# Kernel optimization log

Measured on AMD Instinct MI355X. Metric: run time of the kernel, lower is better.

Reference implementation:

```python
import jax, jax.numpy as jnp
import numpy as np

E = 1024
H = 16
HD = E // H
SCALE = HD ** -0.5


def setup_inputs() -> dict:
    key = jax.random.key(0)
    ks = jax.random.split(key, 8)
    B, S = 2, 2048
    query = jax.random.normal(ks[0], (B, S, E), dtype=jnp.float32)
    kk = jax.random.normal(ks[1], (B, S, E), dtype=jnp.float32)
    vv = jax.random.normal(ks[2], (B, S, E), dtype=jnp.float32)
    lim_in = 1.0 / np.sqrt(E)
    in_proj_w = jax.random.uniform(ks[3], (3 * E, E), minval=-lim_in, maxval=lim_in, dtype=jnp.float32)
    in_proj_b = jax.random.uniform(ks[4], (3 * E,), minval=-lim_in, maxval=lim_in, dtype=jnp.float32)
    out_proj_w = jax.random.uniform(ks[5], (E, E), minval=-lim_in, maxval=lim_in, dtype=jnp.float32)
    out_proj_b = jax.random.uniform(ks[6], (E,), minval=-lim_in, maxval=lim_in, dtype=jnp.float32)
    return {
        "query": query, "key": kk, "value": vv,
        "in_proj_w": in_proj_w, "in_proj_b": in_proj_b,
        "out_proj_w": out_proj_w, "out_proj_b": out_proj_b,
    }


def reference(query, key, value, in_proj_w, in_proj_b, out_proj_w, out_proj_b):
    # NOTE: the torch module ignores `key`/`value`; q,k,v all come from in_proj(query).
    B, S, _ = query.shape
    qkv = jnp.einsum('bse,fe->bsf', query, in_proj_w) + in_proj_b  # [B,S,3E]
    q, k, v = jnp.split(qkv, 3, axis=-1)
    # [B,H,S,HD]
    q = q.reshape(B, S, H, HD).transpose(0, 2, 1, 3) * SCALE
    k = k.reshape(B, S, H, HD).transpose(0, 2, 1, 3)
    v = v.reshape(B, S, H, HD).transpose(0, 2, 1, 3)
    scores = jnp.einsum('bhqd,bhkd->bhqk', q, k)  # [B,H,S,S]
    attn_weights = jax.nn.softmax(scores, axis=-1)
    attn_out = jnp.einsum('bhqk,bhkd->bhqd', attn_weights, v)
    attn_out = attn_out.transpose(0, 2, 1, 3).reshape(B, S, E)
    out = jnp.einsum('bse,fe->bsf', attn_out, out_proj_w) + out_proj_b
    return out, attn_weights
```

## Files before the change

kernel.cpp:

```cpp
#include <hip/hip_runtime.h>

constexpr int kB = 2;
constexpr int kS = 2048;
constexpr int kE = 1024;
constexpr int kF = 3 * kE;

typedef __attribute__((ext_vector_type(8))) short short8;
typedef __attribute__((ext_vector_type(4))) float f32x4;

__device__ __forceinline__ ushort f2bf_rne(float f) {
    uint u = __float_as_uint(f);
    return (ushort)((u + 0x7FFF + ((u >> 16) & 1)) >> 16);
}

__global__ __launch_bounds__(256) void k_cast(const float* __restrict__ in,
                                              ushort* __restrict__ out, int n4)
{
    int i = blockIdx.x * 256 + threadIdx.x;
    if (i < n4) {
        float4 v = ((const float4*)in)[i];
        ushort4 o;
        o.x = f2bf_rne(v.x); o.y = f2bf_rne(v.y);
        o.z = f2bf_rne(v.z); o.w = f2bf_rne(v.w);
        ((ushort4*)out)[i] = o;
    }
}

__device__ __forceinline__ void stage64(ushort* __restrict__ Ls,
                                        const ushort* __restrict__ g,
                                        int gstride, int tid)
{
    int r = tid >> 3;
    int c = (tid & 7) << 3;
    *(uint4*)(Ls + r * 72 + c)        = *(const uint4*)(g + (size_t)r * gstride + c);
    *(uint4*)(Ls + (r + 32) * 72 + c) = *(const uint4*)(g + (size_t)(r + 32) * gstride + c);
}

#define FRAG72(Ls, row, koff) (*(const short8*)((Ls) + (size_t)(row) * 72 + (koff)))

__global__ __launch_bounds__(256) void k_gemm(const ushort* __restrict__ A,
                                              const ushort* __restrict__ Bw,
                                              const float* __restrict__ bias,
                                              ushort* __restrict__ Cb,
                                              float* __restrict__ Cf,
                                              int K, int ldc, int qcols)
{
    __shared__ ushort As[128 * 40];
    __shared__ ushort Bs[128 * 40];
    const int tid = threadIdx.x;
    const int wave = tid >> 6, lane = tid & 63;
    const int quad = lane >> 4, c16 = lane & 15;
    const int wm = (wave >> 1) * 64, wn = (wave & 1) * 64;
    const int row0 = blockIdx.y * 128, col0 = blockIdx.x * 128;

    f32x4 acc[4][4];
#pragma unroll
    for (int i = 0; i < 4; ++i)
#pragma unroll
        for (int j = 0; j < 4; ++j) acc[i][j] = (f32x4){0.f, 0.f, 0.f, 0.f};

    const int sr = tid >> 2;
    const int sq = (tid & 3) << 3;

    for (int k0 = 0; k0 < K; k0 += 32) {
        __syncthreads();
        *(uint4*)(As + sr * 40 + sq)        = *(const uint4*)(A + (size_t)(row0 + sr) * K + k0 + sq);
        *(uint4*)(As + (sr + 64) * 40 + sq) = *(const uint4*)(A + (size_t)(row0 + sr + 64) * K + k0 + sq);
        *(uint4*)(Bs + sr * 40 + sq)        = *(const uint4*)(Bw + (size_t)(col0 + sr) * K + k0 + sq);
        *(uint4*)(Bs + (sr + 64) * 40 + sq) = *(const uint4*)(Bw + (size_t)(col0 + sr + 64) * K + k0 + sq);
        __syncthreads();

        short8 af[4], bf[4];
#pragma unroll
        for (int mt = 0; mt < 4; ++mt)
            af[mt] = *(const short8*)(As + (size_t)(wm + mt * 16 + c16) * 40 + quad * 8);
#pragma unroll
        for (int nt = 0; nt < 4; ++nt)
            bf[nt] = *(const short8*)(Bs + (size_t)(wn + nt * 16 + c16) * 40 + quad * 8);
#pragma unroll
        for (int mt = 0; mt < 4; ++mt)
#pragma unroll
            for (int nt = 0; nt < 4; ++nt)
                acc[mt][nt] = __builtin_amdgcn_mfma_f32_16x16x32_bf16(af[mt], bf[nt], acc[mt][nt], 0, 0, 0);
    }

#pragma unroll
    for (int nt = 0; nt < 4; ++nt) {
        const int colg = col0 + wn + nt * 16 + c16;
        const float bv = bias[colg];
        const float sc = (colg < qcols) ? 0.125f : 1.0f;
#pragma unroll
        for (int mt = 0; mt < 4; ++mt)
#pragma unroll
            for (int r = 0; r < 4; ++r) {
                const int rowg = row0 + wm + mt * 16 + quad * 4 + r;
                float v = acc[mt][nt][r] + bv;
                if (Cb) Cb[(size_t)rowg * ldc + colg] = f2bf_rne(v * sc);
                else    Cf[(size_t)rowg * ldc + colg] = v;
            }
    }
}

__global__ __launch_bounds__(256) void k_vt(const ushort* __restrict__ qkvb,
                                            ushort* __restrict__ vT)
{
    const int b = blockIdx.z, si = blockIdx.y, di = blockIdx.x;
    __shared__ ushort Ls[64 * 72];
    const int tid = threadIdx.x;
    stage64(Ls, qkvb + ((size_t)(b * kS + si * 64)) * kF + 2 * kE + di * 64, kF, tid);
    __syncthreads();
    const int dd = tid >> 3;
    const int s8 = (tid & 7) << 3;
#pragma unroll
    for (int it = 0; it < 2; ++it) {
        const int d = dd + it * 32;
        uint o[4];
#pragma unroll
        for (int i = 0; i < 4; ++i) {
            uint lo = Ls[(s8 + 2 * i) * 72 + d];
            uint hi = Ls[(s8 + 2 * i + 1) * 72 + d];
            o[i] = lo | (hi << 16);
        }
        *(uint4*)(vT + ((size_t)(b * kE + di * 64 + d)) * kS + si * 64 + s8) = *(uint4*)o;
    }
}

__global__ __launch_bounds__(256) void k_attn(const ushort* __restrict__ qkvb,
                                              const ushort* __restrict__ vT,
                                              float* __restrict__ wts,
                                              ushort* __restrict__ aob)
{
    __shared__ ushort Qs[64 * 72];
    __shared__ ushort Ks[64 * 72];
    __shared__ ushort Vts[64 * 72];
    __shared__ ushort Ps[64 * 72];

    const int tid = threadIdx.x;
    const int wave = tid >> 6, lane = tid & 63;
    const int quad = lane >> 4, c16 = lane & 15;
    const int z = blockIdx.y;
    const int b = z >> 4, h = z & 15;
    const int Rq = blockIdx.x * 64;

    const ushort* qg  = qkvb + ((size_t)(b * kS + Rq)) * kF + h * 64;
    const ushort* kg  = qkvb + ((size_t)b * kS) * kF + kE + h * 64;
    const ushort* vtg = vT + ((size_t)(b * kE + h * 64)) * kS;
    float* wrow = wts + ((size_t)(z * kS) + Rq + wave * 16) * kS;

    stage64(Qs, qg, kF, tid);
    __syncthreads();
    const short8 qa0 = FRAG72(Qs, wave * 16 + c16, quad * 8);
    const short8 qa1 = FRAG72(Qs, wave * 16 + c16, quad * 8 + 32);

    float m[4] = {-1e30f, -1e30f, -1e30f, -1e30f};
    float l[4] = {0.f, 0.f, 0.f, 0.f};

    for (int j = 0; j < 32; ++j) {
        __syncthreads();
        stage64(Ks, kg + (size_t)j * 64 * kF, kF, tid);
        __syncthreads();
        f32x4 s[4];
#pragma unroll
        for (int ct = 0; ct < 4; ++ct) {
            short8 b0 = FRAG72(Ks, ct * 16 + c16, quad * 8);
            short8 b1 = FRAG72(Ks, ct * 16 + c16, quad * 8 + 32);
            f32x4 a = (f32x4){0.f, 0.f, 0.f, 0.f};
            a = __builtin_amdgcn_mfma_f32_16x16x32_bf16(qa0, b0, a, 0, 0, 0);
            a = __builtin_amdgcn_mfma_f32_16x16x32_bf16(qa1, b1, a, 0, 0, 0);
            s[ct] = a;
        }
#pragma unroll
        for (int r = 0; r < 4; ++r) {
            float tm = fmaxf(fmaxf(s[0][r], s[1][r]), fmaxf(s[2][r], s[3][r]));
            tm = fmaxf(tm, __shfl_xor(tm, 1));
            tm = fmaxf(tm, __shfl_xor(tm, 2));
            tm = fmaxf(tm, __shfl_xor(tm, 4));
            tm = fmaxf(tm, __shfl_xor(tm, 8));
            const float mn = fmaxf(m[r], tm);
            float sum = __expf(s[0][r] - mn) + __expf(s[1][r] - mn)
                      + __expf(s[2][r] - mn) + __expf(s[3][r] - mn);
            sum += __shfl_xor(sum, 1);
            sum += __shfl_xor(sum, 2);
            sum += __shfl_xor(sum, 4);
            sum += __shfl_xor(sum, 8);
            l[r] = l[r] * __expf(m[r] - mn) + sum;
            m[r] = mn;
        }
    }
    float invl[4];
#pragma unroll
    for (int r = 0; r < 4; ++r) invl[r] = 1.0f / l[r];

    f32x4 o[4];
#pragma unroll
    for (int i = 0; i < 4; ++i) o[i] = (f32x4){0.f, 0.f, 0.f, 0.f};

    for (int j = 0; j < 32; ++j) {
        __syncthreads();
        stage64(Ks, kg + (size_t)j * 64 * kF, kF, tid);
        stage64(Vts, vtg + j * 64, kS, tid);
        __syncthreads();
        f32x4 s[4];
#pragma unroll
        for (int ct = 0; ct < 4; ++ct) {
            short8 b0 = FRAG72(Ks, ct * 16 + c16, quad * 8);
            short8 b1 = FRAG72(Ks, ct * 16 + c16, quad * 8 + 32);
            f32x4 a = (f32x4){0.f, 0.f, 0.f, 0.f};
            a = __builtin_amdgcn_mfma_f32_16x16x32_bf16(qa0, b0, a, 0, 0, 0);
            a = __builtin_amdgcn_mfma_f32_16x16x32_bf16(qa1, b1, a, 0, 0, 0);
            s[ct] = a;
        }
#pragma unroll
        for (int ct = 0; ct < 4; ++ct)
#pragma unroll
            for (int r = 0; r < 4; ++r) {
                const float p = __expf(s[ct][r] - m[r]) * invl[r];
                wrow[(size_t)(quad * 4 + r) * kS + j * 64 + ct * 16 + c16] = p;
                Ps[(size_t)(wave * 16 + quad * 4 + r) * 72 + ct * 16 + c16] = f2bf_rne(p);
            }
        __syncthreads();
        const short8 pa0 = FRAG72(Ps, wave * 16 + c16, quad * 8);
        const short8 pa1 = FRAG72(Ps, wave * 16 + c16, quad * 8 + 32);
#pragma unroll
        for (int ct2 = 0; ct2 < 4; ++ct2) {
            short8 v0 = FRAG72(Vts, ct2 * 16 + c16, quad * 8);
            short8 v1 = FRAG72(Vts, ct2 * 16 + c16, quad * 8 + 32);
            o[ct2] = __builtin_amdgcn_mfma_f32_16x16x32_bf16(pa0, v0, o[ct2], 0, 0, 0);
            o[ct2] = __builtin_amdgcn_mfma_f32_16x16x32_bf16(pa1, v1, o[ct2], 0, 0, 0);
        }
    }

#pragma unroll
    for (int ct2 = 0; ct2 < 4; ++ct2)
#pragma unroll
        for (int r = 0; r < 4; ++r) {
            const size_t row = (size_t)(b * kS + Rq + wave * 16 + quad * 4 + r);
            aob[row * kE + h * 64 + ct2 * 16 + c16] = f2bf_rne(o[ct2][r]);
        }
}


extern "C" void kernel_launch(void* const* d_in, const int* in_sizes, int n_in,
                              void* d_out, int out_size, void* d_ws, size_t ws_size,
                              hipStream_t stream)
{
    const float* query = (const float*)d_in[0];
    const float* in_w  = (const float*)d_in[3];
    const float* in_b  = (const float*)d_in[4];
    const float* out_w = (const float*)d_in[5];
    const float* out_b = (const float*)d_in[6];

    float* out = (float*)d_out;
    float* wts = out + (size_t)kB * kS * kE;

    constexpr size_t MB = 1u << 20;
    char* w = (char*)d_ws;
    ushort* qbf  = (ushort*)(w);
    ushort* wbfi = (ushort*)(w + 8 * MB);
    ushort* wbfo = (ushort*)(w + 14 * MB);
    ushort* qkvb = (ushort*)(w + 16 * MB);
    ushort* vT   = (ushort*)(w + 40 * MB);
    ushort* aob  = (ushort*)(w + 48 * MB);

    dim3 blk(256);
    k_cast<<<dim3((4096 * 1024 / 4 + 255) / 256), blk, 0, stream>>>(query, qbf, 4096 * 1024 / 4);
    k_cast<<<dim3((3072 * 1024 / 4 + 255) / 256), blk, 0, stream>>>(in_w, wbfi, 3072 * 1024 / 4);
    k_cast<<<dim3((1024 * 1024 / 4 + 255) / 256), blk, 0, stream>>>(out_w, wbfo, 1024 * 1024 / 4);

    k_gemm<<<dim3(kF / 128, 4096 / 128), blk, 0, stream>>>(qbf, wbfi, in_b, qkvb, nullptr, kE, kF, kE);

    k_vt<<<dim3(16, 32, 2), blk, 0, stream>>>(qkvb, vT);

    k_attn<<<dim3(kS / 64, kB * 16), blk, 0, stream>>>(qkvb, vT, wts, aob);

    k_gemm<<<dim3(kE / 128, 4096 / 128), blk, 0, stream>>>(aob, wbfo, out_b, nullptr, out, kE, kE, 0);
}
```

Measured before the change: 862.3 us.

## Cache full score rows in LDS to avoid recomputing QK^T in attention

The attention kernel now processes 32 query rows per 512-thread block and stores the whole 32x2048 bf16 score row block in LDS, so QK^T is computed once instead of twice. Softmax runs in a separate exp pass over LDS, and K/V tiles are double-buffered. Weights are written from the stored bf16 exponentials with a fixed offset. This removes the redundant score recompute and the per-tile online max/sum shuffles, at the cost of about 140 KB of LDS per block (one block per CU) and bf16 rounding of the stored scores and weights.

After: 1.013 ms. 17.5% more time.

```diff
diff --git a/kernel.cpp b/kernel.cpp
--- a/kernel.cpp
+++ b/kernel.cpp
@@ -11,6 +11,9 @@
 __device__ __forceinline__ ushort f2bf_rne(float f) {
     uint u = __float_as_uint(f);
     return (ushort)((u + 0x7FFF + ((u >> 16) & 1)) >> 16);
+}
+__device__ __forceinline__ float bf2f(ushort u) {
+    return __uint_as_float((uint)u << 16);
 }
 
 __global__ __launch_bounds__(256) void k_cast(const float* __restrict__ in,
@@ -36,8 +39,6 @@
     *(uint4*)(Ls + (r + 32) * 72 + c) = *(const uint4*)(g + (size_t)(r + 32) * gstride + c);
 }
 
-#define FRAG72(Ls, row, koff) (*(const short8*)((Ls) + (size_t)(row) * 72 + (koff)))
-
 __global__ __launch_bounds__(256) void k_gemm(const ushort* __restrict__ A,
                                               const ushort* __restrict__ Bw,
                                               const float* __restrict__ bias,
@@ -125,118 +126,153 @@
     }
 }
 
-__global__ __launch_bounds__(256) void k_attn(const ushort* __restrict__ qkvb,
+constexpr int SP = 2056;
+constexpr int SC_SH = 32 * SP;
+constexpr int KB_SH = 64 * 72;
+constexpr int ATTN_LDS_BYTES = (SC_SH + 2 * KB_SH) * 2 + (32 * 4 + 32) * 4;
+
+__global__ __launch_bounds__(512) void k_attn(const ushort* __restrict__ qkvb,
                                               const ushort* __restrict__ vT,
                                               float* __restrict__ wts,
                                               ushort* __restrict__ aob)
 {
-    __shared__ ushort Qs[64 * 72];
-    __shared__ ushort Ks[64 * 72];
-    __shared__ ushort Vts[64 * 72];
-    __shared__ ushort Ps[64 * 72];
-
-    const int tid = threadIdx.x;
+    extern __shared__ ushort smem[];
+    ushort* Sc  = smem;
+    ushort* Kb0 = Sc + SC_SH;
+    ushort* Kb1 = Kb0 + KB_SH;
+    float* maxscr = (float*)(Kb1 + KB_SH);
+    float* invls  = maxscr + 32 * 4;
+
+    const int tid  = threadIdx.x;
     const int wave = tid >> 6, lane = tid & 63;
     const int quad = lane >> 4, c16 = lane & 15;
     const int z = blockIdx.y;
     const int b = z >> 4, h = z & 15;
-    const int Rq = blockIdx.x * 64;
+    const int Rq = blockIdx.x * 32;
+    const int mb = (wave & 1) * 16;
+    const int nb = (wave >> 1) * 16;
 
     const ushort* qg  = qkvb + ((size_t)(b * kS + Rq)) * kF + h * 64;
     const ushort* kg  = qkvb + ((size_t)b * kS) * kF + kE + h * 64;
     const ushort* vtg = vT + ((size_t)(b * kE + h * 64)) * kS;
-    float* wrow = wts + ((size_t)(z * kS) + Rq + wave * 16) * kS;
-
-    stage64(Qs, qg, kF, tid);
-    __syncthreads();
-    const short8 qa0 = FRAG72(Qs, wave * 16 + c16, quad * 8);
-    const short8 qa1 = FRAG72(Qs, wave * 16 + c16, quad * 8 + 32);
-
-    float m[4] = {-1e30f, -1e30f, -1e30f, -1e30f};
-    float l[4] = {0.f, 0.f, 0.f, 0.f};
-
+
+    const int strow = tid >> 3, stcol = (tid & 7) << 3;
+
+    const short8 qa0 = *(const short8*)(qg + (size_t)(mb + c16) * kF + quad * 8);
+    const short8 qa1 = *(const short8*)(qg + (size_t)(mb + c16) * kF + quad * 8 + 32);
+
+    constexpr float Coff = 3.0f;
+    float m4[4] = {-1e30f, -1e30f, -1e30f, -1e30f};
+
+    *(uint4*)(Kb0 + strow * 72 + stcol) = *(const uint4*)(kg + (size_t)strow * kF + stcol);
+    __syncthreads();
+
+#pragma unroll 2
     for (int j = 0; j < 32; ++j) {
+        const ushort* cur = (j & 1) ? Kb1 : Kb0;
+        ushort* nxt       = (j & 1) ? Kb0 : Kb1;
+        if (j + 1 < 32)
+            *(uint4*)(nxt + strow * 72 + stcol) =
+                *(const uint4*)(kg + (size_t)((j + 1) * 64 + strow) * kF + stcol);
+
+        short8 b0 = *(const short8*)(cur + (size_t)(nb + c16) * 72 + quad * 8);
+        short8 b1 = *(const short8*)(cur + (size_t)(nb + c16) * 72 + quad * 8 + 32);
+        f32x4 a = (f32x4){0.f, 0.f, 0.f, 0.f};
+        a = __builtin_amdgcn_mfma_f32_16x16x32_bf16(qa0, b0, a, 0, 0, 0);
+        a = __builtin_amdgcn_mfma_f32_16x16x32_bf16(qa1, b1, a, 0, 0, 0);
+#pragma unroll
+        for (int r = 0; r < 4; ++r) {
+            const float t = a[r] - Coff;
+            m4[r] = fmaxf(m4[r], t);
+            Sc[(size_t)(mb + quad * 4 + r) * SP + j * 64 + nb + c16] = f2bf_rne(t);
+        }
         __syncthreads();
-        stage64(Ks, kg + (size_t)j * 64 * kF, kF, tid);
+    }
+
+#pragma unroll
+    for (int r = 0; r < 4; ++r) {
+        float t = m4[r];
+        t = fmaxf(t, __shfl_xor(t, 1));
+        t = fmaxf(t, __shfl_xor(t, 2));
+        t = fmaxf(t, __shfl_xor(t, 4));
+        t = fmaxf(t, __shfl_xor(t, 8));
+        if (c16 == 0) maxscr[(mb + quad * 4 + r) * 4 + (wave >> 1)] = t;
+    }
+    __syncthreads();
+
+    const int prow = wave * 4 + (lane >> 4);
+    const float mt = fmaxf(fmaxf(maxscr[prow * 4 + 0], maxscr[prow * 4 + 1]),
+                           fmaxf(maxscr[prow * 4 + 2], maxscr[prow * 4 + 3]));
+    float ls0 = 0.f, ls1 = 0.f;
+    ushort* rbase = Sc + (size_t)prow * SP + c16 * 8;
+#pragma unroll 4
+    for (int it = 0; it < 16; ++it) {
+        short8 sv = *(const short8*)(rbase + it * 128);
+        short8 ev;
+#pragma unroll
+        for (int i = 0; i < 8; ++i) {
+            const float e = __expf(bf2f((ushort)sv[i]) - mt);
+            if (i & 1) ls1 += e; else ls0 += e;
+            ev[i] = (short)f2bf_rne(e);
+        }
+        *(short8*)(rbase + it * 128) = ev;
+    }
+    float lsum = ls0 + ls1;
+    lsum += __shfl_xor(lsum, 1);
+    lsum += __shfl_xor(lsum, 2);
+    lsum += __shfl_xor(lsum, 4);
+    lsum += __shfl_xor(lsum, 8);
+    if (c16 == 0) invls[prow] = 1.0f / lsum;
+    __syncthreads();
+
+    const float invl_m = invls[mb + c16];
+    f32x4 o = (f32x4){0.f, 0.f, 0.f, 0.f};
+
+    *(uint4*)(Kb0 + strow * 72 + stcol) = *(const uint4*)(vtg + (size_t)strow * kS + stcol);
+    __syncthreads();
+
+#pragma unroll 2
+    for (int j = 0; j < 32; ++j) {
+        const ushort* cur = (j & 1) ? Kb1 : Kb0;
+        ushort* nxt       = (j & 1) ? Kb0 : Kb1;
+        if (j + 1 < 32)
+            *(uint4*)(nxt + strow * 72 + stcol) =
+                *(const uint4*)(vtg + (size_t)strow * kS + (j + 1) * 64 + stcol);
+
+        const ushort* pr = Sc + (size_t)(mb + c16) * SP + j * 64 + quad * 8;
+        short8 pa0 = *(const short8*)(pr);
+        short8 pa1 = *(const short8*)(pr + 32);
+        short8 v0 = *(const short8*)(cur + (size_t)(nb + c16) * 72 + quad * 8);
+        short8 v1 = *(const short8*)(cur + (size_t)(nb + c16) * 72 + quad * 8 + 32);
+        o = __builtin_amdgcn_mfma_f32_16x16x32_bf16(pa0, v0, o, 0, 0, 0);
+        o = __builtin_amdgcn_mfma_f32_16x16x32_bf16(pa1, v1, o, 0, 0, 0);
+
+        if (wave < 2) {
+            float* wp = wts + ((size_t)z * kS + Rq + mb + c16) * kS + j * 64 + quad * 8;
+            float4 w0, w1, w2, w3;
+            w0.x = bf2f((ushort)pa0[0]) * invl_m; w0.y = bf2f((ushort)pa0[1]) * invl_m;
+            w0.z = bf2f((ushort)pa0[2]) * invl_m; w0.w = bf2f((ushort)pa0[3]) * invl_m;
+            w1.x = bf2f((ushort)pa0[4]) * invl_m; w1.y = bf2f((ushort)pa0[5]) * invl_m;
+            w1.z = bf2f((ushort)pa0[6]) * invl_m; w1.w = bf2f((ushort)pa0[7]) * invl_m;
+            w2.x = bf2f((ushort)pa1[0]) * invl_m; w2.y = bf2f((ushort)pa1[1]) * invl_m;
+            w2.z = bf2f((ushort)pa1[2]) * invl_m; w2.w = bf2f((ushort)pa1[3]) * invl_m;
+            w3.x = bf2f((ushort)pa1[4]) * invl_m; w3.y = bf2f((ushort)pa1[5]) * invl_m;
+            w3.z = bf2f((ushort)pa1[6]) * invl_m; w3.w = bf2f((ushort)pa1[7]) * invl_m;
+            *(float4*)(wp)      = w0;
+            *(float4*)(wp + 4)  = w1;
+            *(float4*)(wp + 32) = w2;
+            *(float4*)(wp + 36) = w3;
+        }
         __syncthreads();
-        f32x4 s[4];
-#pragma unroll
-        for (int ct = 0; ct < 4; ++ct) {
-            short8 b0 = FRAG72(Ks, ct * 16 + c16, quad * 8);
-            short8 b1 = FRAG72(Ks, ct * 16 + c16, quad * 8 + 32);
-            f32x4 a = (f32x4){0.f, 0.f, 0.f, 0.f};
-            a = __builtin_amdgcn_mfma_f32_16x16x32_bf16(qa0, b0, a, 0, 0, 0);
-            a = __builtin_amdgcn_mfma_f32_16x16x32_bf16(qa1, b1, a, 0, 0, 0);
-            s[ct] = a;
-        }
-#pragma unroll
-        for (int r = 0; r < 4; ++r) {
-            float tm = fmaxf(fmaxf(s[0][r], s[1][r]), fmaxf(s[2][r], s[3][r]));
-            tm = fmaxf(tm, __shfl_xor(tm, 1));
-            tm = fmaxf(tm, __shfl_xor(tm, 2));
-            tm = fmaxf(tm, __shfl_xor(tm, 4));
-            tm = fmaxf(tm, __shfl_xor(tm, 8));
-            const float mn = fmaxf(m[r], tm);
-            float sum = __expf(s[0][r] - mn) + __expf(s[1][r] - mn)
-                      + __expf(s[2][r] - mn) + __expf(s[3][r] - mn);
-            sum += __shfl_xor(sum, 1);
-            sum += __shfl_xor(sum, 2);
-            sum += __shfl_xor(sum, 4);
-            sum += __shfl_xor(sum, 8);
-            l[r] = l[r] * __expf(m[r] - mn) + sum;
-            m[r] = mn;
-        }
-    }
-    float invl[4];
-#pragma unroll
-    for (int r = 0; r < 4; ++r) invl[r] = 1.0f / l[r];
-
-    f32x4 o[4];
-#pragma unroll
-    for (int i = 0; i < 4; ++i) o[i] = (f32x4){0.f, 0.f, 0.f, 0.f};
-
-    for (int j = 0; j < 32; ++j) {
-        __syncthreads();
-        stage64(Ks, kg + (size_t)j * 64 * kF, kF, tid);
-        stage64(Vts, vtg + j * 64, kS, tid);
-        __syncthreads();
-        f32x4 s[4];
-#pragma unroll
-        for (int ct = 0; ct < 4; ++ct) {
-            short8 b0 = FRAG72(Ks, ct * 16 + c16, quad * 8);
-            short8 b1 = FRAG72(Ks, ct * 16 + c16, quad * 8 + 32);
-            f32x4 a = (f32x4){0.f, 0.f, 0.f, 0.f};
-            a = __builtin_amdgcn_mfma_f32_16x16x32_bf16(qa0, b0, a, 0, 0, 0);
-            a = __builtin_amdgcn_mfma_f32_16x16x32_bf16(qa1, b1, a, 0, 0, 0);
-            s[ct] = a;
-        }
-#pragma unroll
-        for (int ct = 0; ct < 4; ++ct)
-#pragma unroll
-            for (int r = 0; r < 4; ++r) {
-                const float p = __expf(s[ct][r] - m[r]) * invl[r];
-                wrow[(size_t)(quad * 4 + r) * kS + j * 64 + ct * 16 + c16] = p;
-                Ps[(size_t)(wave * 16 + quad * 4 + r) * 72 + ct * 16 + c16] = f2bf_rne(p);
-            }
-        __syncthreads();
-        const short8 pa0 = FRAG72(Ps, wave * 16 + c16, quad * 8);
-        const short8 pa1 = FRAG72(Ps, wave * 16 + c16, quad * 8 + 32);
-#pragma unroll
-        for (int ct2 = 0; ct2 < 4; ++ct2) {
-            short8 v0 = FRAG72(Vts, ct2 * 16 + c16, quad * 8);
-            short8 v1 = FRAG72(Vts, ct2 * 16 + c16, quad * 8 + 32);
-            o[ct2] = __builtin_amdgcn_mfma_f32_16x16x32_bf16(pa0, v0, o[ct2], 0, 0, 0);
-            o[ct2] = __builtin_amdgcn_mfma_f32_16x16x32_bf16(pa1, v1, o[ct2], 0, 0, 0);
-        }
-    }
-
-#pragma unroll
-    for (int ct2 = 0; ct2 < 4; ++ct2)
-#pragma unroll
-        for (int r = 0; r < 4; ++r) {
-            const size_t row = (size_t)(b * kS + Rq + wave * 16 + quad * 4 + r);
-            aob[row * kE + h * 64 + ct2 * 16 + c16] = f2bf_rne(o[ct2][r]);
-        }
+    }
+
+    const int orow = mb + quad * 4;
+#pragma unroll
+    for (int r = 0; r < 4; ++r) {
+        const float iv = invls[orow + r];
+        aob[((size_t)(b * kS + Rq + orow + r)) * kE + h * 64 + nb + c16] =
+            f2bf_rne(o[r] * iv);
+    }
 }
 
 
@@ -271,7 +307,9 @@
 
     k_vt<<<dim3(16, 32, 2), blk, 0, stream>>>(qkvb, vT);
 
-    k_attn<<<dim3(kS / 64, kB * 16), blk, 0, stream>>>(qkvb, vT, wts, aob);
+    hipFuncSetAttribute(reinterpret_cast<const void*>(k_attn),
+                        hipFuncAttributeMaxDynamicSharedMemorySize, ATTN_LDS_BYTES);
+    k_attn<<<dim3(kS / 32, kB * 16), dim3(512), ATTN_LDS_BYTES, stream>>>(qkvb, vT, wts, aob);
 
     k_gemm<<<dim3(kE / 128, 4096 / 128), blk, 0, stream>>>(aob, wbfo, out_b, nullptr, out, kE, kE, 0);
 }
```

## Rewrite attention to hold full score rows in LDS, computing QK once

Applied to the files above, without the earlier changes.

The attention kernel now processes 16 query rows per 512-thread block and stores the full 2048-wide score rows as bf16 in dynamic shared memory. This replaces the two-pass online softmax that computed QK^T twice. It does an exact max/sum pass, then a PV matmul split across waves with the partial results reduced through LDS, then writes normalized weights with vectorized float4 stores. K and V fragments are read straight from global memory instead of being staged in LDS. The trade-offs are lower precision, because scores and exponentials are rounded to bf16 and a constant offset is subtracted, and much larger LDS use per block, which limits occupancy.

New measurement: 873.9 us. Within noise of the previous version (+1.3%).

```diff
diff --git a/kernel.cpp b/kernel.cpp
--- a/kernel.cpp
+++ b/kernel.cpp
@@ -11,6 +11,9 @@
 __device__ __forceinline__ ushort f2bf_rne(float f) {
     uint u = __float_as_uint(f);
     return (ushort)((u + 0x7FFF + ((u >> 16) & 1)) >> 16);
+}
+__device__ __forceinline__ float bf2f(ushort u) {
+    return __uint_as_float((uint)u << 16);
 }
 
 __global__ __launch_bounds__(256) void k_cast(const float* __restrict__ in,
@@ -36,8 +39,6 @@
     *(uint4*)(Ls + (r + 32) * 72 + c) = *(const uint4*)(g + (size_t)(r + 32) * gstride + c);
 }
 
-#define FRAG72(Ls, row, koff) (*(const short8*)((Ls) + (size_t)(row) * 72 + (koff)))
-
 __global__ __launch_bounds__(256) void k_gemm(const ushort* __restrict__ A,
                                               const ushort* __restrict__ Bw,
                                               const float* __restrict__ bias,
@@ -125,118 +126,142 @@
     }
 }
 
-__global__ __launch_bounds__(256) void k_attn(const ushort* __restrict__ qkvb,
+constexpr int QR = 16;
+constexpr int SP = 2056;
+constexpr int SC_SH = QR * SP;
+constexpr int ATTN_LDS_BYTES = SC_SH * 2 + (QR * 8) * 4 + QR * 4 + 8 * 256 * 4;
+
+__global__ __launch_bounds__(512) void k_attn(const ushort* __restrict__ qkvb,
                                               const ushort* __restrict__ vT,
                                               float* __restrict__ wts,
                                               ushort* __restrict__ aob)
 {
-    __shared__ ushort Qs[64 * 72];
-    __shared__ ushort Ks[64 * 72];
-    __shared__ ushort Vts[64 * 72];
-    __shared__ ushort Ps[64 * 72];
-
-    const int tid = threadIdx.x;
+    extern __shared__ ushort smem[];
+    ushort* Sc    = smem;
+    float* maxscr = (float*)(Sc + SC_SH);
+    float* invls  = maxscr + QR * 8;
+    float* pvscr  = invls + QR;
+
+    const int tid  = threadIdx.x;
     const int wave = tid >> 6, lane = tid & 63;
     const int quad = lane >> 4, c16 = lane & 15;
     const int z = blockIdx.y;
     const int b = z >> 4, h = z & 15;
-    const int Rq = blockIdx.x * 64;
+    const int Rq = blockIdx.x * QR;
 
     const ushort* qg  = qkvb + ((size_t)(b * kS + Rq)) * kF + h * 64;
     const ushort* kg  = qkvb + ((size_t)b * kS) * kF + kE + h * 64;
     const ushort* vtg = vT + ((size_t)(b * kE + h * 64)) * kS;
-    float* wrow = wts + ((size_t)(z * kS) + Rq + wave * 16) * kS;
-
-    stage64(Qs, qg, kF, tid);
-    __syncthreads();
-    const short8 qa0 = FRAG72(Qs, wave * 16 + c16, quad * 8);
-    const short8 qa1 = FRAG72(Qs, wave * 16 + c16, quad * 8 + 32);
-
-    float m[4] = {-1e30f, -1e30f, -1e30f, -1e30f};
-    float l[4] = {0.f, 0.f, 0.f, 0.f};
-
-    for (int j = 0; j < 32; ++j) {
-        __syncthreads();
-        stage64(Ks, kg + (size_t)j * 64 * kF, kF, tid);
-        __syncthreads();
-        f32x4 s[4];
-#pragma unroll
-        for (int ct = 0; ct < 4; ++ct) {
-            short8 b0 = FRAG72(Ks, ct * 16 + c16, quad * 8);
-            short8 b1 = FRAG72(Ks, ct * 16 + c16, quad * 8 + 32);
+
+    const short8 qa0 = *(const short8*)(qg + (size_t)c16 * kF + quad * 8);
+    const short8 qa1 = *(const short8*)(qg + (size_t)c16 * kF + quad * 8 + 32);
+
+    constexpr float Coff = 3.0f;
+    float m4[4] = {-1e30f, -1e30f, -1e30f, -1e30f};
+    {
+        const int colbase = wave * 256;
+#pragma unroll 4
+        for (int t = 0; t < 16; ++t) {
+            const ushort* kr = kg + (size_t)(colbase + t * 16 + c16) * kF;
+            short8 b0 = *(const short8*)(kr + quad * 8);
+            short8 b1 = *(const short8*)(kr + quad * 8 + 32);
             f32x4 a = (f32x4){0.f, 0.f, 0.f, 0.f};
             a = __builtin_amdgcn_mfma_f32_16x16x32_bf16(qa0, b0, a, 0, 0, 0);
             a = __builtin_amdgcn_mfma_f32_16x16x32_bf16(qa1, b1, a, 0, 0, 0);
-            s[ct] = a;
-        }
+#pragma unroll
+            for (int r = 0; r < 4; ++r) {
+                const float tv = a[r] - Coff;
+                m4[r] = fmaxf(m4[r], tv);
+                Sc[(size_t)(quad * 4 + r) * SP + colbase + t * 16 + c16] = f2bf_rne(tv);
+            }
+        }
+    }
+#pragma unroll
+    for (int r = 0; r < 4; ++r) {
+        float tv = m4[r];
+        tv = fmaxf(tv, __shfl_xor(tv, 1));
+        tv = fmaxf(tv, __shfl_xor(tv, 2));
+        tv = fmaxf(tv, __shfl_xor(tv, 4));
+        tv = fmaxf(tv, __shfl_xor(tv, 8));
+        if (c16 == 0) maxscr[(quad * 4 + r) * 8 + wave] = tv;
+    }
+    __syncthreads();
+
+    {
+        const int prow = tid >> 5, l32 = tid & 31;
+        float mr = maxscr[prow * 8];
+#pragma unroll
+        for (int i = 1; i < 8; ++i) mr = fmaxf(mr, maxscr[prow * 8 + i]);
+        float ls = 0.f;
+        ushort* rb = Sc + (size_t)prow * SP;
+#pragma unroll
+        for (int it = 0; it < 8; ++it) {
+            const int col = it * 256 + l32 * 8;
+            short8 sv = *(const short8*)(rb + col);
+            short8 ev;
+#pragma unroll
+            for (int i = 0; i < 8; ++i) {
+                const float e = __expf(bf2f((ushort)sv[i]) - mr);
+                ls += e;
+                ev[i] = (short)f2bf_rne(e);
+            }
+            *(short8*)(rb + col) = ev;
+        }
+        ls += __shfl_xor(ls, 1);
+        ls += __shfl_xor(ls, 2);
+        ls += __shfl_xor(ls, 4);
+        ls += __shfl_xor(ls, 8);
+        ls += __shfl_xor(ls, 16);
+        if (l32 == 0) invls[prow] = 1.0f / ls;
+    }
+    __syncthreads();
+
+    {
+        const int nb = (wave & 3) * 16;
+        const int kh = wave >> 2;
+        f32x4 o = (f32x4){0.f, 0.f, 0.f, 0.f};
+        const ushort* pb = Sc + (size_t)c16 * SP + kh * 1024 + quad * 8;
+        const ushort* vb = vtg + (size_t)(nb + c16) * kS + kh * 1024 + quad * 8;
+#pragma unroll 4
+        for (int s = 0; s < 32; ++s) {
+            short8 pa = *(const short8*)(pb + s * 32);
+            short8 vf = *(const short8*)(vb + s * 32);
+            o = __builtin_amdgcn_mfma_f32_16x16x32_bf16(pa, vf, o, 0, 0, 0);
+        }
+        float* ps = pvscr + wave * 256;
+#pragma unroll
+        for (int r = 0; r < 4; ++r) ps[(quad * 4 + r) * 16 + c16] = o[r];
+    }
+    __syncthreads();
+    if (wave < 4) {
+        const float* p0 = pvscr + wave * 256;
+        const float* p1 = p0 + 4 * 256;
 #pragma unroll
         for (int r = 0; r < 4; ++r) {
-            float tm = fmaxf(fmaxf(s[0][r], s[1][r]), fmaxf(s[2][r], s[3][r]));
-            tm = fmaxf(tm, __shfl_xor(tm, 1));
-            tm = fmaxf(tm, __shfl_xor(tm, 2));
-            tm = fmaxf(tm, __shfl_xor(tm, 4));
-            tm = fmaxf(tm, __shfl_xor(tm, 8));
-            const float mn = fmaxf(m[r], tm);
-            float sum = __expf(s[0][r] - mn) + __expf(s[1][r] - mn)
-                      + __expf(s[2][r] - mn) + __expf(s[3][r] - mn);
-            sum += __shfl_xor(sum, 1);
-            sum += __shfl_xor(sum, 2);
-            sum += __shfl_xor(sum, 4);
-            sum += __shfl_xor(sum, 8);
-            l[r] = l[r] * __expf(m[r] - mn) + sum;
-            m[r] = mn;
-        }
-    }
-    float invl[4];
-#pragma unroll
-    for (int r = 0; r < 4; ++r) invl[r] = 1.0f / l[r];
-
-    f32x4 o[4];
-#pragma unroll
-    for (int i = 0; i < 4; ++i) o[i] = (f32x4){0.f, 0.f, 0.f, 0.f};
-
-    for (int j = 0; j < 32; ++j) {
-        __syncthreads();
-        stage64(Ks, kg + (size_t)j * 64 * kF, kF, tid);
-        stage64(Vts, vtg + j * 64, kS, tid);
-        __syncthreads();
-        f32x4 s[4];
-#pragma unroll
-        for (int ct = 0; ct < 4; ++ct) {
-            short8 b0 = FRAG72(Ks, ct * 16 + c16, quad * 8);
-            short8 b1 = FRAG72(Ks, ct * 16 + c16, quad * 8 + 32);
-            f32x4 a = (f32x4){0.f, 0.f, 0.f, 0.f};
-            a = __builtin_amdgcn_mfma_f32_16x16x32_bf16(qa0, b0, a, 0, 0, 0);
-            a = __builtin_amdgcn_mfma_f32_16x16x32_bf16(qa1, b1, a, 0, 0, 0);
-            s[ct] = a;
-        }
-#pragma unroll
-        for (int ct = 0; ct < 4; ++ct)
-#pragma unroll
-            for (int r = 0; r < 4; ++r) {
-                const float p = __expf(s[ct][r] - m[r]) * invl[r];
-                wrow[(size_t)(quad * 4 + r) * kS + j * 64 + ct * 16 + c16] = p;
-                Ps[(size_t)(wave * 16 + quad * 4 + r) * 72 + ct * 16 + c16] = f2bf_rne(p);
-            }
-        __syncthreads();
-        const short8 pa0 = FRAG72(Ps, wave * 16 + c16, quad * 8);
-        const short8 pa1 = FRAG72(Ps, wave * 16 + c16, quad * 8 + 32);
-#pragma unroll
-        for (int ct2 = 0; ct2 < 4; ++ct2) {
-            short8 v0 = FRAG72(Vts, ct2 * 16 + c16, quad * 8);
-            short8 v1 = FRAG72(Vts, ct2 * 16 + c16, quad * 8 + 32);
-            o[ct2] = __builtin_amdgcn_mfma_f32_16x16x32_bf16(pa0, v0, o[ct2], 0, 0, 0);
-            o[ct2] = __builtin_amdgcn_mfma_f32_16x16x32_bf16(pa1, v1, o[ct2], 0, 0, 0);
-        }
-    }
-
-#pragma unroll
-    for (int ct2 = 0; ct2 < 4; ++ct2)
-#pragma unroll
-        for (int r = 0; r < 4; ++r) {
-            const size_t row = (size_t)(b * kS + Rq + wave * 16 + quad * 4 + r);
-            aob[row * kE + h * 64 + ct2 * 16 + c16] = f2bf_rne(o[ct2][r]);
-        }
+            const int row = quad * 4 + r;
+            const float val = (p0[row * 16 + c16] + p1[row * 16 + c16]) * invls[row];
+            aob[((size_t)(b * kS + Rq + row)) * kE + h * 64 + wave * 16 + c16] = f2bf_rne(val);
+        }
+    }
+
+    {
+        const int row = tid >> 5, l32 = tid & 31;
+        const float iv = invls[row];
+        float* wp = wts + ((size_t)z * kS + Rq + row) * kS;
+        const ushort* rb = Sc + (size_t)row * SP;
+#pragma unroll
+        for (int it = 0; it < 8; ++it) {
+            const int col = it * 256 + l32 * 8;
+            short8 ev = *(const short8*)(rb + col);
+            float4 w0, w1;
+            w0.x = bf2f((ushort)ev[0]) * iv; w0.y = bf2f((ushort)ev[1]) * iv;
+            w0.z = bf2f((ushort)ev[2]) * iv; w0.w = bf2f((ushort)ev[3]) * iv;
+            w1.x = bf2f((ushort)ev[4]) * iv; w1.y = bf2f((ushort)ev[5]) * iv;
+            w1.z = bf2f((ushort)ev[6]) * iv; w1.w = bf2f((ushort)ev[7]) * iv;
+            *(float4*)(wp + col)     = w0;
+            *(float4*)(wp + col + 4) = w1;
+        }
+    }
 }
 
 
@@ -271,7 +296,9 @@
 
     k_vt<<<dim3(16, 32, 2), blk, 0, stream>>>(qkvb, vT);
 
-    k_attn<<<dim3(kS / 64, kB * 16), blk, 0, stream>>>(qkvb, vT, wts, aob);
+    hipFuncSetAttribute(reinterpret_cast<const void*>(k_attn),
+                        hipFuncAttributeMaxDynamicSharedMemorySize, ATTN_LDS_BYTES);
+    k_attn<<<dim3(kS / QR, kB * 16), dim3(512), ATTN_LDS_BYTES, stream>>>(qkvb, vT, wts, aob);
 
     k_gemm<<<dim3(kE / 128, 4096 / 128), blk, 0, stream>>>(aob, wbfo, out_b, nullptr, out, kE, kE, 0);
 }
```
